# Kernel optimization log

Measured on AMD Instinct MI355X. Metric: run time of the kernel, lower is better.

The kernel has to match this reference:

```python
import jax, jax.numpy as jnp
import numpy as np

N = 2_000_000
C = 64
B = 16
H = C // 2  # reduction_ratio = 2


def setup_inputs() -> dict:
    key = jax.random.key(0)
    k1, k2, k3, k4, k5, k6 = jax.random.split(key, 6)
    x = jax.random.normal(k1, (N, C), dtype=jnp.float32)
    batch_ids = jnp.sort(jax.random.randint(k2, (N,), 0, B, dtype=jnp.int32))
    # nn.Linear-style params: y = x @ W.T + b
    W1 = jax.random.normal(k3, (H, C), dtype=jnp.float32) * (1.0 / np.sqrt(C))
    b1 = jax.random.normal(k4, (H,), dtype=jnp.float32) * 0.01
    W2 = jax.random.normal(k5, (C, H), dtype=jnp.float32) * (1.0 / np.sqrt(H))
    b2 = jax.random.normal(k6, (C,), dtype=jnp.float32) * 0.01
    return {"x": x, "batch_ids": batch_ids, "W1": W1, "b1": b1, "W2": W2, "b2": b2}


def reference(x, batch_ids, W1, b1, W2, b2):
    # Global avg / max pooling per batch segment -> [B, C]
    sums = jax.ops.segment_sum(x, batch_ids, num_segments=B)
    counts = jax.ops.segment_sum(jnp.ones((x.shape[0],), x.dtype), batch_ids, num_segments=B)
    avg = sums / jnp.maximum(counts, 1.0)[:, None]
    mx = jax.ops.segment_max(x, batch_ids, num_segments=B)

    def mlp(h):  # shared tiny MLP: Linear -> ReLU -> Linear
        return jax.nn.relu(h @ W1.T + b1) @ W2.T + b2

    att = jax.nn.sigmoid(mlp(avg) + mlp(mx))  # [B, C]
    # per-point broadcast multiply-add: x * att[batch] + x
    return x * att[batch_ids] + x
```

## Files before the change

kernel.cpp:

```cpp
#include <hip/hip_runtime.h>
#include <math.h>

#define NCH   64
#define NBAT  16
#define NHID  32
#define NBLK  1024

typedef float f4 __attribute__((ext_vector_type(4)));


__device__ __forceinline__ void atomicMaxF(float* addr, float v) {
    if (v >= 0.0f) atomicMax((int*)addr, __float_as_int(v));
    else           atomicMin((unsigned int*)addr, __float_as_uint(v));
}

__global__ __launch_bounds__(256) void init_kernel(float* ws) {
    int i = blockIdx.x * blockDim.x + threadIdx.x;
    if (i < 1024) {
        ws[i] = 0.0f;
        ws[1024 + i] = -INFINITY;
    }
    if (i < NBAT) ws[2048 + i] = 0.0f;
}

__device__ __forceinline__ void flush_seg(float* __restrict__ wsum,
                                          float* __restrict__ wmax,
                                          float* __restrict__ wcnt,
                                          int b, int c4,
                                          const float4& s, const float4& m, float cnt) {
    float* ps = wsum + b * NCH + c4 * 4;
    atomicAdd(ps + 0, s.x);
    atomicAdd(ps + 1, s.y);
    atomicAdd(ps + 2, s.z);
    atomicAdd(ps + 3, s.w);
    float* pm = wmax + b * NCH + c4 * 4;
    atomicMaxF(pm + 0, m.x);
    atomicMaxF(pm + 1, m.y);
    atomicMaxF(pm + 2, m.z);
    atomicMaxF(pm + 3, m.w);
    if (c4 == 0) atomicAdd(wcnt + b, cnt);
}

__global__ __launch_bounds__(256) void pool_kernel(const float* __restrict__ x,
                                                   const int* __restrict__ bid,
                                                   float* __restrict__ wsum,
                                                   float* __restrict__ wmax,
                                                   float* __restrict__ wcnt,
                                                   int n, int rpb) {
    const int tid = threadIdx.x;
    const int c4 = tid & 15;
    const int rg = tid >> 4;
    const int r0 = blockIdx.x * rpb;
    const int rend = min(r0 + rpb, n);

    int cur = -1;
    float4 s = make_float4(0.f, 0.f, 0.f, 0.f);
    float4 m = make_float4(-INFINITY, -INFINITY, -INFINITY, -INFINITY);
    float cnt = 0.0f;

    for (int r = r0 + rg; r < rend; r += 16) {
        int b = bid[r];
        if (b != cur) {
            if (cur >= 0) flush_seg(wsum, wmax, wcnt, cur, c4, s, m, cnt);
            cur = b;
            s = make_float4(0.f, 0.f, 0.f, 0.f);
            m = make_float4(-INFINITY, -INFINITY, -INFINITY, -INFINITY);
            cnt = 0.0f;
        }
        const float4 v = *reinterpret_cast<const float4*>(x + (size_t)r * NCH + c4 * 4);
        s.x += v.x; s.y += v.y; s.z += v.z; s.w += v.w;
        m.x = fmaxf(m.x, v.x); m.y = fmaxf(m.y, v.y);
        m.z = fmaxf(m.z, v.z); m.w = fmaxf(m.w, v.w);
        cnt += 1.0f;
    }

    __shared__ int    lb[256];
    __shared__ float4 ls[256];
    __shared__ float4 lm[256];
    __shared__ float  lc[256];
    lb[tid] = cur; ls[tid] = s; lm[tid] = m; lc[tid] = cnt;
    __syncthreads();
    if (rg == 0) {
        for (int g = 1; g < 16; ++g) {
            int i = g * 16 + c4;
            int ob = lb[i];
            if (ob < 0) continue;
            if (ob == cur && cur >= 0) {
                const float4 os = ls[i]; const float4 om = lm[i];
                s.x += os.x; s.y += os.y; s.z += os.z; s.w += os.w;
                m.x = fmaxf(m.x, om.x); m.y = fmaxf(m.y, om.y);
                m.z = fmaxf(m.z, om.z); m.w = fmaxf(m.w, om.w);
                cnt += lc[i];
            } else if (cur < 0) {
                cur = ob; s = ls[i]; m = lm[i]; cnt = lc[i];
            } else {
                flush_seg(wsum, wmax, wcnt, ob, c4, ls[i], lm[i], lc[i]);
            }
        }
        if (cur >= 0) flush_seg(wsum, wmax, wcnt, cur, c4, s, m, cnt);
    }
}

__global__ __launch_bounds__(512) void mlp_kernel(const float* __restrict__ ws,
                                                  const float* __restrict__ W1,
                                                  const float* __restrict__ b1,
                                                  const float* __restrict__ W2,
                                                  const float* __restrict__ b2,
                                                  float* __restrict__ scale_out) {
    __shared__ float avg[NBAT * NCH];
    __shared__ float mxs[NBAT * NCH];
    __shared__ float h1a[NBAT * NHID];
    __shared__ float h1m[NBAT * NHID];
    const int t = threadIdx.x;

    for (int i = t; i < NBAT * NCH; i += 512) {
        float c = ws[2048 + (i >> 6)];
        avg[i] = ws[i] / fmaxf(c, 1.0f);
        mxs[i] = ws[1024 + i];
    }
    __syncthreads();

    {
        const int b = t >> 5, j = t & 31;
        float sa = b1[j], sm = b1[j];
        const float* w = W1 + j * NCH;
        for (int c = 0; c < NCH; ++c) {
            float wv = w[c];
            sa += avg[b * NCH + c] * wv;
            sm += mxs[b * NCH + c] * wv;
        }
        h1a[b * NHID + j] = fmaxf(sa, 0.0f);
        h1m[b * NHID + j] = fmaxf(sm, 0.0f);
    }
    __syncthreads();

    for (int i = t; i < NBAT * NCH; i += 512) {
        const int b = i >> 6, c = i & 63;
        float ya = b2[c], ym = b2[c];
        const float* w = W2 + c * NHID;
        for (int j = 0; j < NHID; ++j) {
            float wv = w[j];
            ya += h1a[b * NHID + j] * wv;
            ym += h1m[b * NHID + j] * wv;
        }
        float z = ya + ym;
        float sig = 1.0f / (1.0f + expf(-z));
        scale_out[i] = 1.0f + sig;
    }
}

__global__ __launch_bounds__(256) void apply_kernel(const float* __restrict__ x,
                                                    const int* __restrict__ bid,
                                                    const float* __restrict__ scale,
                                                    float* __restrict__ out,
                                                    int n, int rpb) {
    __shared__ float s_scale[NBAT * NCH];
    for (int i = threadIdx.x; i < NBAT * NCH; i += 256) s_scale[i] = scale[i];
    __syncthreads();

    const int r0 = blockIdx.x * rpb;
    const int rend = min(r0 + rpb, n);
    const int c4 = threadIdx.x & 15;
    const int rg = threadIdx.x >> 4;
    const int base = r0 + rg;
    if (base >= rend) return;

    const int iters = (rend - base + 15) >> 4;
    for (int k = iters - 1; k >= 0; --k) {
        const int r = base + (k << 4);
        const int b = bid[r];
        const f4 v  = *reinterpret_cast<const f4*>(x + (size_t)r * NCH + c4 * 4);
        const f4 sc = *reinterpret_cast<const f4*>(s_scale + b * NCH + c4 * 4);
        const f4 o = v * sc;
        __builtin_nontemporal_store(o, reinterpret_cast<f4*>(out + (size_t)r * NCH + c4 * 4));
    }
}

extern "C" void kernel_launch(void* const* d_in, const int* in_sizes, int n_in,
                              void* d_out, int out_size, void* d_ws, size_t ws_size,
                              hipStream_t stream) {
    const float* x   = (const float*)d_in[0];
    const int*   bid = (const int*)d_in[1];
    const float* W1  = (const float*)d_in[2];
    const float* b1  = (const float*)d_in[3];
    const float* W2  = (const float*)d_in[4];
    const float* b2  = (const float*)d_in[5];
    float* out = (float*)d_out;
    const int n = in_sizes[1];

    float* ws     = (float*)d_ws;
    float* wsum   = ws;
    float* wmax   = ws + 1024;
    float* wcnt   = ws + 2048;
    float* wscale = ws + 2064;

    hipLaunchKernelGGL(init_kernel, dim3(4), dim3(256), 0, stream, ws);

    const int rpb = (n + NBLK - 1) / NBLK;
    hipLaunchKernelGGL(pool_kernel, dim3(NBLK), dim3(256), 0, stream,
                       x, bid, wsum, wmax, wcnt, n, rpb);

    hipLaunchKernelGGL(mlp_kernel, dim3(1), dim3(512), 0, stream,
                       ws, W1, b1, W2, b2, wscale);

    hipLaunchKernelGGL(apply_kernel, dim3(NBLK), dim3(256), 0, stream,
                       x, bid, wscale, out, n, rpb);
}
```

Measured before the change: 317.4 us.

## Split apply kernel into four sub-blocks per pool chunk with 2x unrolled loop

The apply kernel launches four times as many blocks. Each pool-kernel chunk is split into four sub-ranges, assigned in reverse order so the last-touched (likely cache-resident) rows are read first, and the row loop is unrolled by two to keep more loads in flight. The aim is better occupancy and memory-level parallelism in the bandwidth-bound broadcast multiply. In exchange, each block reloads the 4KB scale table, and with four times as many blocks that adds small per-block overhead.

```diff
diff --git a/kernel.cpp b/kernel.cpp
--- a/kernel.cpp
+++ b/kernel.cpp
@@ -5,6 +5,7 @@
 #define NBAT  16
 #define NHID  32
 #define NBLK  1024
+#define NSUB  4
 
 typedef float f4 __attribute__((ext_vector_type(4)));
 
@@ -153,21 +154,34 @@
                                                     const int* __restrict__ bid,
                                                     const float* __restrict__ scale,
                                                     float* __restrict__ out,
-                                                    int n, int rpb) {
+                                                    int n, int rpb, int rps) {
     __shared__ float s_scale[NBAT * NCH];
     for (int i = threadIdx.x; i < NBAT * NCH; i += 256) s_scale[i] = scale[i];
     __syncthreads();
 
-    const int r0 = blockIdx.x * rpb;
+    const int pc  = blockIdx.x & (NBLK - 1);
+    const int sub = (NSUB - 1) - (blockIdx.x >> 10);
+    const int r0   = pc * rpb;
     const int rend = min(r0 + rpb, n);
+    const int lo = r0 + sub * rps;
+    const int hi = min(lo + rps, rend);
     const int c4 = threadIdx.x & 15;
     const int rg = threadIdx.x >> 4;
-    const int base = r0 + rg;
-    if (base >= rend) return;
-
-    const int iters = (rend - base + 15) >> 4;
-    for (int k = iters - 1; k >= 0; --k) {
-        const int r = base + (k << 4);
+
+    int r = lo + rg;
+    for (; r + 16 < hi; r += 32) {
+        const int b0 = bid[r];
+        const int b1 = bid[r + 16];
+        const f4 v0 = *reinterpret_cast<const f4*>(x + (size_t)r * NCH + c4 * 4);
+        const f4 v1 = *reinterpret_cast<const f4*>(x + (size_t)(r + 16) * NCH + c4 * 4);
+        const f4 s0 = *reinterpret_cast<const f4*>(s_scale + b0 * NCH + c4 * 4);
+        const f4 s1 = *reinterpret_cast<const f4*>(s_scale + b1 * NCH + c4 * 4);
+        const f4 o0 = v0 * s0;
+        const f4 o1 = v1 * s1;
+        __builtin_nontemporal_store(o0, reinterpret_cast<f4*>(out + (size_t)r * NCH + c4 * 4));
+        __builtin_nontemporal_store(o1, reinterpret_cast<f4*>(out + (size_t)(r + 16) * NCH + c4 * 4));
+    }
+    if (r < hi) {
         const int b = bid[r];
         const f4 v  = *reinterpret_cast<const f4*>(x + (size_t)r * NCH + c4 * 4);
         const f4 sc = *reinterpret_cast<const f4*>(s_scale + b * NCH + c4 * 4);
@@ -203,6 +217,7 @@
     hipLaunchKernelGGL(mlp_kernel, dim3(1), dim3(512), 0, stream,
                        ws, W1, b1, W2, b2, wscale);
 
-    hipLaunchKernelGGL(apply_kernel, dim3(NBLK), dim3(256), 0, stream,
-                       x, bid, wscale, out, n, rpb);
-}
+    const int rps = (rpb + NSUB - 1) / NSUB;
+    hipLaunchKernelGGL(apply_kernel, dim3(NBLK * NSUB), dim3(256), 0, stream,
+                       x, bid, wscale, out, n, rpb, rps);
+}
```

Measured after the change: 323.9 us. +2.0%, slower.

## Use binary-searched segment boundaries instead of per-row batch ids

Applied to the files above, without the earlier changes.

Because batch_ids are sorted, each block binary-searches the start of every segment and then loops over segments, so the per-row batch id reads and per-row branch checks in the pool and apply kernels go away. Counts are computed from the boundaries in the MLP kernel, which removes the count atomics. The inner loops are unrolled by four to keep more loads in flight. This adds a binary search per block and a per-segment sync loop in the pool kernel, and it depends on the ids being sorted.

```diff
diff --git a/kernel.cpp b/kernel.cpp
--- a/kernel.cpp
+++ b/kernel.cpp
@@ -14,107 +14,114 @@
     else           atomicMin((unsigned int*)addr, __float_as_uint(v));
 }
 
+__device__ __forceinline__ f4 vmax4(f4 a, f4 b) {
+    f4 r;
+    r.x = fmaxf(a.x, b.x); r.y = fmaxf(a.y, b.y);
+    r.z = fmaxf(a.z, b.z); r.w = fmaxf(a.w, b.w);
+    return r;
+}
+
+__device__ __forceinline__ int lower_bound_i(const int* __restrict__ a, int n, int v) {
+    int lo = 0, hi = n;
+    while (lo < hi) {
+        const int mid = (lo + hi) >> 1;
+        if (a[mid] < v) lo = mid + 1; else hi = mid;
+    }
+    return lo;
+}
+
 __global__ __launch_bounds__(256) void init_kernel(float* ws) {
-    int i = blockIdx.x * blockDim.x + threadIdx.x;
+    const int i = blockIdx.x * blockDim.x + threadIdx.x;
     if (i < 1024) {
         ws[i] = 0.0f;
         ws[1024 + i] = -INFINITY;
     }
-    if (i < NBAT) ws[2048 + i] = 0.0f;
-}
-
-__device__ __forceinline__ void flush_seg(float* __restrict__ wsum,
-                                          float* __restrict__ wmax,
-                                          float* __restrict__ wcnt,
-                                          int b, int c4,
-                                          const float4& s, const float4& m, float cnt) {
-    float* ps = wsum + b * NCH + c4 * 4;
-    atomicAdd(ps + 0, s.x);
-    atomicAdd(ps + 1, s.y);
-    atomicAdd(ps + 2, s.z);
-    atomicAdd(ps + 3, s.w);
-    float* pm = wmax + b * NCH + c4 * 4;
-    atomicMaxF(pm + 0, m.x);
-    atomicMaxF(pm + 1, m.y);
-    atomicMaxF(pm + 2, m.z);
-    atomicMaxF(pm + 3, m.w);
-    if (c4 == 0) atomicAdd(wcnt + b, cnt);
 }
 
 __global__ __launch_bounds__(256) void pool_kernel(const float* __restrict__ x,
                                                    const int* __restrict__ bid,
                                                    float* __restrict__ wsum,
                                                    float* __restrict__ wmax,
-                                                   float* __restrict__ wcnt,
                                                    int n, int rpb) {
-    const int tid = threadIdx.x;
-    const int c4 = tid & 15;
-    const int rg = tid >> 4;
+    __shared__ int sstart[NBAT + 1];
+    __shared__ f4 ls[256];
+    __shared__ f4 lm[256];
+    const int t = threadIdx.x;
+    if (t <= NBAT) sstart[t] = (t == NBAT) ? n : lower_bound_i(bid, n, t);
+    __syncthreads();
+
+    const int c4 = t & 15;
+    const int rg = t >> 4;
     const int r0 = blockIdx.x * rpb;
     const int rend = min(r0 + rpb, n);
-
-    int cur = -1;
-    float4 s = make_float4(0.f, 0.f, 0.f, 0.f);
-    float4 m = make_float4(-INFINITY, -INFINITY, -INFINITY, -INFINITY);
-    float cnt = 0.0f;
-
-    for (int r = r0 + rg; r < rend; r += 16) {
-        int b = bid[r];
-        if (b != cur) {
-            if (cur >= 0) flush_seg(wsum, wmax, wcnt, cur, c4, s, m, cnt);
-            cur = b;
-            s = make_float4(0.f, 0.f, 0.f, 0.f);
-            m = make_float4(-INFINITY, -INFINITY, -INFINITY, -INFINITY);
-            cnt = 0.0f;
-        }
-        const float4 v = *reinterpret_cast<const float4*>(x + (size_t)r * NCH + c4 * 4);
-        s.x += v.x; s.y += v.y; s.z += v.z; s.w += v.w;
-        m.x = fmaxf(m.x, v.x); m.y = fmaxf(m.y, v.y);
-        m.z = fmaxf(m.z, v.z); m.w = fmaxf(m.w, v.w);
-        cnt += 1.0f;
-    }
-
-    __shared__ int    lb[256];
-    __shared__ float4 ls[256];
-    __shared__ float4 lm[256];
-    __shared__ float  lc[256];
-    lb[tid] = cur; ls[tid] = s; lm[tid] = m; lc[tid] = cnt;
-    __syncthreads();
-    if (rg == 0) {
-        for (int g = 1; g < 16; ++g) {
-            int i = g * 16 + c4;
-            int ob = lb[i];
-            if (ob < 0) continue;
-            if (ob == cur && cur >= 0) {
-                const float4 os = ls[i]; const float4 om = lm[i];
-                s.x += os.x; s.y += os.y; s.z += os.z; s.w += os.w;
-                m.x = fmaxf(m.x, om.x); m.y = fmaxf(m.y, om.y);
-                m.z = fmaxf(m.z, om.z); m.w = fmaxf(m.w, om.w);
-                cnt += lc[i];
-            } else if (cur < 0) {
-                cur = ob; s = ls[i]; m = lm[i]; cnt = lc[i];
-            } else {
-                flush_seg(wsum, wmax, wcnt, ob, c4, ls[i], lm[i], lc[i]);
+    const f4 fzero = {0.f, 0.f, 0.f, 0.f};
+    const f4 fninf = {-INFINITY, -INFINITY, -INFINITY, -INFINITY};
+
+    for (int b = 0; b < NBAT; ++b) {
+        const int lo = max(sstart[b], r0);
+        const int hi = min(sstart[b + 1], rend);
+        if (lo >= hi) continue;
+
+        f4 s = fzero, m = fninf;
+        const int base = lo + rg;
+        const int k = (hi > base) ? ((hi - base + 15) >> 4) : 0;
+        const float* xp = x + (size_t)base * NCH + c4 * 4;
+        int j = 0;
+        for (; j + 4 <= k; j += 4) {
+            const f4 v0 = *reinterpret_cast<const f4*>(xp + (size_t)(j + 0) * 16 * NCH);
+            const f4 v1 = *reinterpret_cast<const f4*>(xp + (size_t)(j + 1) * 16 * NCH);
+            const f4 v2 = *reinterpret_cast<const f4*>(xp + (size_t)(j + 2) * 16 * NCH);
+            const f4 v3 = *reinterpret_cast<const f4*>(xp + (size_t)(j + 3) * 16 * NCH);
+            s += v0; s += v1; s += v2; s += v3;
+            m = vmax4(m, vmax4(vmax4(v0, v1), vmax4(v2, v3)));
+        }
+        for (; j < k; ++j) {
+            const f4 v = *reinterpret_cast<const f4*>(xp + (size_t)j * 16 * NCH);
+            s += v; m = vmax4(m, v);
+        }
+
+        ls[t] = s; lm[t] = m;
+        __syncthreads();
+        if (rg == 0) {
+            for (int gg = 1; gg < 16; ++gg) {
+                s += ls[gg * 16 + c4];
+                m = vmax4(m, lm[gg * 16 + c4]);
             }
-        }
-        if (cur >= 0) flush_seg(wsum, wmax, wcnt, cur, c4, s, m, cnt);
+            float* ps = wsum + b * NCH + c4 * 4;
+            atomicAdd(ps + 0, s.x);
+            atomicAdd(ps + 1, s.y);
+            atomicAdd(ps + 2, s.z);
+            atomicAdd(ps + 3, s.w);
+            float* pm = wmax + b * NCH + c4 * 4;
+            atomicMaxF(pm + 0, m.x);
+            atomicMaxF(pm + 1, m.y);
+            atomicMaxF(pm + 2, m.z);
+            atomicMaxF(pm + 3, m.w);
+        }
+        __syncthreads();
     }
 }
 
 __global__ __launch_bounds__(512) void mlp_kernel(const float* __restrict__ ws,
+                                                  const int* __restrict__ bid,
                                                   const float* __restrict__ W1,
                                                   const float* __restrict__ b1,
                                                   const float* __restrict__ W2,
                                                   const float* __restrict__ b2,
-                                                  float* __restrict__ scale_out) {
+                                                  float* __restrict__ scale_out,
+                                                  int n) {
+    __shared__ int   sstart[NBAT + 1];
     __shared__ float avg[NBAT * NCH];
     __shared__ float mxs[NBAT * NCH];
     __shared__ float h1a[NBAT * NHID];
     __shared__ float h1m[NBAT * NHID];
     const int t = threadIdx.x;
+    if (t <= NBAT) sstart[t] = (t == NBAT) ? n : lower_bound_i(bid, n, t);
+    __syncthreads();
 
     for (int i = t; i < NBAT * NCH; i += 512) {
-        float c = ws[2048 + (i >> 6)];
+        const int b = i >> 6;
+        const float c = (float)(sstart[b + 1] - sstart[b]);
         avg[i] = ws[i] / fmaxf(c, 1.0f);
         mxs[i] = ws[1024 + i];
     }
@@ -125,7 +132,7 @@
         float sa = b1[j], sm = b1[j];
         const float* w = W1 + j * NCH;
         for (int c = 0; c < NCH; ++c) {
-            float wv = w[c];
+            const float wv = w[c];
             sa += avg[b * NCH + c] * wv;
             sm += mxs[b * NCH + c] * wv;
         }
@@ -139,12 +146,12 @@
         float ya = b2[c], ym = b2[c];
         const float* w = W2 + c * NHID;
         for (int j = 0; j < NHID; ++j) {
-            float wv = w[j];
+            const float wv = w[j];
             ya += h1a[b * NHID + j] * wv;
             ym += h1m[b * NHID + j] * wv;
         }
-        float z = ya + ym;
-        float sig = 1.0f / (1.0f + expf(-z));
+        const float z = ya + ym;
+        const float sig = 1.0f / (1.0f + expf(-z));
         scale_out[i] = 1.0f + sig;
     }
 }
@@ -154,25 +161,45 @@
                                                     const float* __restrict__ scale,
                                                     float* __restrict__ out,
                                                     int n, int rpb) {
+    __shared__ int   sstart[NBAT + 1];
     __shared__ float s_scale[NBAT * NCH];
-    for (int i = threadIdx.x; i < NBAT * NCH; i += 256) s_scale[i] = scale[i];
-    __syncthreads();
-
+    const int t = threadIdx.x;
+    if (t <= NBAT) sstart[t] = (t == NBAT) ? n : lower_bound_i(bid, n, t);
+    for (int i = t; i < NBAT * NCH; i += 256) s_scale[i] = scale[i];
+    __syncthreads();
+
+    const int c4 = t & 15;
+    const int rg = t >> 4;
     const int r0 = blockIdx.x * rpb;
     const int rend = min(r0 + rpb, n);
-    const int c4 = threadIdx.x & 15;
-    const int rg = threadIdx.x >> 4;
-    const int base = r0 + rg;
-    if (base >= rend) return;
-
-    const int iters = (rend - base + 15) >> 4;
-    for (int k = iters - 1; k >= 0; --k) {
-        const int r = base + (k << 4);
-        const int b = bid[r];
-        const f4 v  = *reinterpret_cast<const f4*>(x + (size_t)r * NCH + c4 * 4);
+
+    for (int b = NBAT - 1; b >= 0; --b) {
+        const int lo = max(sstart[b], r0);
+        const int hi = min(sstart[b + 1], rend);
+        if (lo >= hi) continue;
+
         const f4 sc = *reinterpret_cast<const f4*>(s_scale + b * NCH + c4 * 4);
-        const f4 o = v * sc;
-        __builtin_nontemporal_store(o, reinterpret_cast<f4*>(out + (size_t)r * NCH + c4 * 4));
+        const int base = lo + rg;
+        int k = (hi > base) ? ((hi - base + 15) >> 4) : 0;
+        const float* xp = x + (size_t)base * NCH + c4 * 4;
+        float* op = out + (size_t)base * NCH + c4 * 4;
+
+        while (k >= 4) {
+            k -= 4;
+            const f4 v0 = *reinterpret_cast<const f4*>(xp + (size_t)(k + 0) * 16 * NCH);
+            const f4 v1 = *reinterpret_cast<const f4*>(xp + (size_t)(k + 1) * 16 * NCH);
+            const f4 v2 = *reinterpret_cast<const f4*>(xp + (size_t)(k + 2) * 16 * NCH);
+            const f4 v3 = *reinterpret_cast<const f4*>(xp + (size_t)(k + 3) * 16 * NCH);
+            __builtin_nontemporal_store(v0 * sc, reinterpret_cast<f4*>(op + (size_t)(k + 0) * 16 * NCH));
+            __builtin_nontemporal_store(v1 * sc, reinterpret_cast<f4*>(op + (size_t)(k + 1) * 16 * NCH));
+            __builtin_nontemporal_store(v2 * sc, reinterpret_cast<f4*>(op + (size_t)(k + 2) * 16 * NCH));
+            __builtin_nontemporal_store(v3 * sc, reinterpret_cast<f4*>(op + (size_t)(k + 3) * 16 * NCH));
+        }
+        while (k > 0) {
+            --k;
+            const f4 v = *reinterpret_cast<const f4*>(xp + (size_t)k * 16 * NCH);
+            __builtin_nontemporal_store(v * sc, reinterpret_cast<f4*>(op + (size_t)k * 16 * NCH));
+        }
     }
 }
 
@@ -191,17 +218,16 @@
     float* ws     = (float*)d_ws;
     float* wsum   = ws;
     float* wmax   = ws + 1024;
-    float* wcnt   = ws + 2048;
     float* wscale = ws + 2064;
 
     hipLaunchKernelGGL(init_kernel, dim3(4), dim3(256), 0, stream, ws);
 
     const int rpb = (n + NBLK - 1) / NBLK;
     hipLaunchKernelGGL(pool_kernel, dim3(NBLK), dim3(256), 0, stream,
-                       x, bid, wsum, wmax, wcnt, n, rpb);
+                       x, bid, wsum, wmax, n, rpb);
 
     hipLaunchKernelGGL(mlp_kernel, dim3(1), dim3(512), 0, stream,
-                       ws, W1, b1, W2, b2, wscale);
+                       ws, bid, W1, b1, W2, b2, wscale, n);
 
     hipLaunchKernelGGL(apply_kernel, dim3(NBLK), dim3(256), 0, stream,
                        x, bid, wscale, out, n, rpb);
```

Result: faster. 302.3 us, median of 2 (-4.8%).
